# Optimization experiments

Hardware: AMD Instinct MI355X
Metric: run time of the kernel (lower is better)

The kernel has to match this reference:

```python
import jax, jax.numpy as jnp
import numpy as np

B, S, E, H = 2, 2048, 1024, 16
D = E // H


def setup_inputs() -> dict:
    key = jax.random.key(0)
    ks = jax.random.split(key, 8)
    q = jax.random.normal(ks[0], (B, S, E), dtype=jnp.float32)
    k = jax.random.normal(ks[1], (B, S, E), dtype=jnp.float32)
    v = jax.random.normal(ks[2], (B, S, E), dtype=jnp.float32)
    mask = jax.random.randint(ks[3], (B, 1, 1, S), 0, 2, dtype=jnp.int32)
    sc = 1.0 / np.sqrt(E)
    W_qkv = jax.random.normal(ks[4], (3 * E, E), dtype=jnp.float32) * sc
    b_qkv = jnp.zeros((3 * E,), dtype=jnp.float32)
    W_out = jax.random.normal(ks[5], (E, E), dtype=jnp.float32) * sc
    b_out = jnp.zeros((E,), dtype=jnp.float32)
    return {"q": q, "k": k, "v": v, "mask": mask,
            "W_qkv": W_qkv, "b_qkv": b_qkv, "W_out": W_out, "b_out": b_out}


def reference(q, k, v, mask, W_qkv, b_qkv, W_out, b_out):
    # Fused qkv linear: q takes the Q-slice, k the K-slice, v the V-slice.
    qp = (q @ W_qkv[:E].T + b_qkv[:E]).reshape(B, S, H, D)
    kp = (k @ W_qkv[E:2 * E].T + b_qkv[E:2 * E]).reshape(B, S, H, D)
    vp = (v @ W_qkv[2 * E:].T + b_qkv[2 * E:]).reshape(B, S, H, D)
    # (B,H,S,S) scores -- NOTE: original module does NOT scale by sqrt(d)
    energy = jnp.einsum('nqhd,nkhd->nhqk', qp, kp)
    energy = jnp.where(mask == 0, jnp.float32(-1e20), energy)
    attention = jax.nn.softmax(energy, axis=-1)
    out = jnp.einsum('nhql,nlhd->nqhd', attention, vp).reshape(B, S, E)
    return out @ W_out.T + b_out
```

## Files before the change

### kernel.cpp

```cpp
#include <hip/hip_runtime.h>
#include <stdint.h>

constexpr int B_ = 2, S_ = 2048, E_ = 1024, H_ = 16, D_ = 64;
constexpr int M_ = B_ * S_;

typedef unsigned short u16;
typedef __attribute__((ext_vector_type(8))) short short8;
typedef __attribute__((ext_vector_type(4))) float f32x4;

__device__ __forceinline__ u16 f2bf(float f) {
  uint32_t u = __float_as_uint(f);
  return (u16)((u + 0x7FFFu + ((u >> 16) & 1u)) >> 16);
}
__device__ __forceinline__ void tsplit(float x, u16& hi, u16& lo) {
  const uint32_t u = __float_as_uint(x);
  hi = (u16)(u >> 16);
  const float hif = __uint_as_float(u & 0xFFFF0000u);
  lo = (u16)(__float_as_uint(x - hif) >> 16);
}

__device__ __forceinline__ void block_sync() {
  asm volatile("s_waitcnt lgkmcnt(0)" ::: "memory");
  __builtin_amdgcn_s_barrier();
}

__global__ __launch_bounds__(256) void split_f32_kernel(
    const float* __restrict__ src, u16* __restrict__ hi, u16* __restrict__ lo, int n4)
{
  const int i = blockIdx.x * 256 + threadIdx.x;
  if (i >= n4) return;
  const float4 x = ((const float4*)src)[i];
  ushort4 h, l;
  tsplit(x.x, h.x, l.x); tsplit(x.y, h.y, l.y);
  tsplit(x.z, h.z, l.z); tsplit(x.w, h.w, l.w);
  ((ushort4*)hi)[i] = h;
  ((ushort4*)lo)[i] = l;
}

__global__ __launch_bounds__(256) void mask_scan_kernel(
    const int* __restrict__ mask, int* __restrict__ opos, int* __restrict__ nk)
{
  __shared__ int tmp[256];
  __shared__ int coff;
  const int b = blockIdx.x, t = threadIdx.x;
  for (int c = t; c < S_; c += 256) opos[b * S_ + c] = 0;
  if (t == 0) coff = 0;
  __syncthreads();
  for (int c = 0; c < S_; c += 256) {
    const int m = (mask[b * S_ + c + t] != 0) ? 1 : 0;
    int x = m;
    tmp[t] = x;
    __syncthreads();
#pragma unroll
    for (int off = 1; off < 256; off <<= 1) {
      const int v = (t >= off) ? tmp[t - off] : 0;
      __syncthreads();
      x += v;
      tmp[t] = x;
      __syncthreads();
    }
    const int base = coff;
    if (m) opos[b * S_ + base + x - 1] = c + t;
    __syncthreads();
    if (t == 255) coff = base + x;
    __syncthreads();
  }
  if (t == 0) nk[b] = coff;
}

__global__ __launch_bounds__(256) void gemm_qkv_kernel(
    const float* __restrict__ q, const float* __restrict__ k, const float* __restrict__ v,
    const u16* __restrict__ WHi, const u16* __restrict__ WLo,
    const float* __restrict__ bias,
    const int* __restrict__ Opos, const int* __restrict__ NkArr,
    u16* __restrict__ QpHi, u16* __restrict__ QpLo,
    u16* __restrict__ KpHi, u16* __restrict__ KpLo,
    u16* __restrict__ Vp)
{
  __shared__ __align__(16) short smem[15360];
  short* Ah = smem;
  short* Al = smem + 5120;
  short* Bh = smem + 10240;
  short* Bl = smem + 12800;

  const int t = threadIdx.x;
  const int m0 = blockIdx.x * 128;
  const int n0g = blockIdx.y * 64;
  const int proj = n0g >> 10;
  const int nloc = n0g & (E_ - 1);
  const bool split = (proj < 2);
  const int bb = m0 >> 11, mloc = m0 & (S_ - 1);
  const int nkb = NkArr[bb];
  if (proj != 0 && mloc >= nkb) return;

  const float* A = (proj == 0) ? q : (proj == 1) ? k : v;

  const int w = t >> 6, lane = t & 63;
  const int g = lane >> 4, lc = lane & 15;
  const int wm = w & 1, wn = w >> 1;
  const int sra = t >> 1, sca = (t & 1) * 16;
  const int srb = t >> 2, scb = (t & 3) * 8;

  int arow;
  if (proj == 0) arow = m0 + sra;
  else arow = bb * S_ + (Opos[bb * S_ + mloc + sra] & (S_ - 1));
  const float* Abp = A + (size_t)arow * E_ + sca;
  const u16* Bhb = WHi + (size_t)(n0g + srb) * E_ + scb;
  const u16* Blb = WLo + (size_t)(n0g + srb) * E_ + scb;

  f32x4 acc[4][2];
#pragma unroll
  for (int i = 0; i < 4; ++i)
#pragma unroll
    for (int j = 0; j < 2; ++j) acc[i][j] = (f32x4){0.f, 0.f, 0.f, 0.f};

  auto loadA = [&](float4* ar, int kk) {
#pragma unroll
    for (int i = 0; i < 4; ++i) ar[i] = *(const float4*)(Abp + kk + 4 * i);
  };
  auto writeA = [&](const float4* ar) {
    ushort hh[16], ll[16];
#pragma unroll
    for (int i = 0; i < 4; ++i) {
      tsplit(ar[i].x, hh[4 * i + 0], ll[4 * i + 0]);
      tsplit(ar[i].y, hh[4 * i + 1], ll[4 * i + 1]);
      tsplit(ar[i].z, hh[4 * i + 2], ll[4 * i + 2]);
      tsplit(ar[i].w, hh[4 * i + 3], ll[4 * i + 3]);
    }
    *(short8*)&Ah[sra * 40 + sca]     = *(const short8*)&hh[0];
    *(short8*)&Ah[sra * 40 + sca + 8] = *(const short8*)&hh[8];
    if (split) {
      *(short8*)&Al[sra * 40 + sca]     = *(const short8*)&ll[0];
      *(short8*)&Al[sra * 40 + sca + 8] = *(const short8*)&ll[8];
    }
  };

  float4 arP[2][4];
  short8 brP[2], crP[2] = {};
  loadA(arP[0], 0);
  loadA(arP[1], 32);
  brP[0] = *(const short8*)(Bhb);
  brP[1] = *(const short8*)(Bhb + 32);
  if (split) {
    crP[0] = *(const short8*)(Blb);
    crP[1] = *(const short8*)(Blb + 32);
  }

#pragma unroll 2
  for (int k0 = 0; k0 < E_; k0 += 32) {
    const int p = (k0 >> 5) & 1;
    block_sync();
    writeA(arP[p]);
    *(short8*)&Bh[srb * 40 + scb] = brP[p];
    if (split) *(short8*)&Bl[srb * 40 + scb] = crP[p];
    block_sync();
    {
      const int kk = (k0 + 64) & (E_ - 1);
      loadA(arP[p], kk);
      brP[p] = *(const short8*)(Bhb + kk);
      if (split) crP[p] = *(const short8*)(Blb + kk);
    }

    short8 ah[4], al[4], bh[2], bl[2];
#pragma unroll
    for (int mt = 0; mt < 4; ++mt) {
      const int ro = (wm * 64 + mt * 16 + lc) * 40 + g * 8;
      ah[mt] = *(const short8*)&Ah[ro];
      if (split) al[mt] = *(const short8*)&Al[ro];
    }
#pragma unroll
    for (int nt = 0; nt < 2; ++nt) {
      const int ro = (wn * 32 + nt * 16 + lc) * 40 + g * 8;
      bh[nt] = *(const short8*)&Bh[ro];
      if (split) bl[nt] = *(const short8*)&Bl[ro];
    }
#pragma unroll
    for (int mt = 0; mt < 4; ++mt)
#pragma unroll
      for (int nt = 0; nt < 2; ++nt) {
        f32x4 a = acc[mt][nt];
        a = __builtin_amdgcn_mfma_f32_16x16x32_bf16(ah[mt], bh[nt], a, 0, 0, 0);
        if (split) {
          a = __builtin_amdgcn_mfma_f32_16x16x32_bf16(ah[mt], bl[nt], a, 0, 0, 0);
          a = __builtin_amdgcn_mfma_f32_16x16x32_bf16(al[mt], bh[nt], a, 0, 0, 0);
        }
        acc[mt][nt] = a;
      }
  }

  float bs[2];
#pragma unroll
  for (int nt = 0; nt < 2; ++nt) bs[nt] = bias[n0g + wn * 32 + nt * 16 + lc];

  if (proj < 2) {
    u16* Hi = (proj == 0) ? QpHi : KpHi;
    u16* Lo = (proj == 0) ? QpLo : KpLo;
    const int head = nloc >> 6;
    short* T = smem + w * 2560;
    const int s = (m0 + wm * 64 + lane) & (S_ - 1);
    const size_t rowb = (((size_t)(bb * H_ + head)) * S_ + s) * D_ + wn * 32;
#pragma unroll
    for (int pass = 0; pass < 2; ++pass) {
      __syncthreads();
#pragma unroll
      for (int nt = 0; nt < 2; ++nt)
#pragma unroll
        for (int mt = 0; mt < 4; ++mt)
#pragma unroll
          for (int r = 0; r < 4; ++r) {
            const float val = acc[mt][nt][r] + bs[nt];
            const uint32_t u = __float_as_uint(val);
            u16 x;
            if (pass == 0) x = (u16)(u >> 16);
            else {
              const float hif = __uint_as_float(u & 0xFFFF0000u);
              x = (u16)(__float_as_uint(val - hif) >> 16);
            }
            T[(mt * 16 + g * 4 + r) * 40 + nt * 16 + lc] = (short)x;
          }
      __syncthreads();
      u16* dst = (pass == 0) ? Hi : Lo;
#pragma unroll
      for (int j = 0; j < 4; ++j)
        *(short8*)&dst[rowb + 8 * j] = *(const short8*)&T[lane * 40 + 8 * j];
    }
  } else {
#pragma unroll
    for (int mt = 0; mt < 4; ++mt) {
      const int jb = mloc + wm * 64 + mt * 16 + g * 4;
#pragma unroll
      for (int nt = 0; nt < 2; ++nt) {
        const int nE = nloc + wn * 32 + nt * 16 + lc;
        const int h = nE >> 6, d = nE & 63;
        const size_t rb = (((size_t)(bb * H_ + h)) * D_ + d) * S_;
#pragma unroll
        for (int r = 0; r < 4; ++r) {
          if (jb + r < nkb) Vp[rb + jb + r] = f2bf(acc[mt][nt][r] + bs[nt]);
        }
      }
    }
  }
}

__global__ __launch_bounds__(256, 4) void attn_mfma_kernel(
    const u16* __restrict__ QpHi, const u16* __restrict__ QpLo,
    const u16* __restrict__ KpHi, const u16* __restrict__ KpLo,
    const u16* __restrict__ Vp,
    const int* __restrict__ nkArr,
    u16* __restrict__ AOHi)
{
  __shared__ __align__(16) short sm[18432];
  short* Khi = sm;
  short* Klo = sm + 4608;
  short* Vt  = sm + 9216;
  short* Pb  = sm + 13824;

  const int t = threadIdx.x;
  const int w = t >> 6, lane = t & 63;
  const int g = lane >> 4, lc = lane & 15;
  const int bh = blockIdx.y;
  const int b = bh >> 4, hh = bh & 15;
  const int q0 = blockIdx.x * 64;
  const size_t hb = (size_t)bh * S_ * D_;
  const u16* QgH = QpHi + hb;
  const u16* QgL = QpLo + hb;
  const u16* KgH = KpHi + hb;
  const u16* KgL = KpLo + hb;
  const u16* Vg  = Vp + hb;
  short* Pw = Pb + w * 1152;

  const int nk = nkArr[b];
  const int kend = ((nk + 63) >> 6) << 6;

  short8 qh[2], ql[2];
  {
    const size_t base = (size_t)(q0 + 16 * w + lc) * D_ + 8 * g;
    qh[0] = *(const short8*)&QgH[base];
    qh[1] = *(const short8*)&QgH[base + 32];
    ql[0] = *(const short8*)&QgL[base];
    ql[1] = *(const short8*)&QgL[base + 32];
  }

  short8 ones8 = {0, 0, 0, 0, 0, 0, 0, 0};
  if (lc == 0) {
    const short o = (short)0x3F80;
    ones8 = (short8){o, o, o, o, o, o, o, o};
  }

  f32x4 O[4];
  f32x4 Ol = (f32x4){0.f, 0.f, 0.f, 0.f};
#pragma unroll
  for (int dt = 0; dt < 4; ++dt) O[dt] = (f32x4){0.f, 0.f, 0.f, 0.f};
  float mst[4] = {-INFINITY, -INFINITY, -INFINITY, -INFINITY};

  const int srow = t >> 2, sc16 = (t & 3) * 16;

  short8 kr[2], lr[2], vr[2];
  kr[0] = *(const short8*)&KgH[srow * D_ + sc16];
  kr[1] = *(const short8*)&KgH[srow * D_ + sc16 + 8];
  lr[0] = *(const short8*)&KgL[srow * D_ + sc16];
  lr[1] = *(const short8*)&KgL[srow * D_ + sc16 + 8];
  vr[0] = *(const short8*)&Vg[srow * S_ + sc16];
  vr[1] = *(const short8*)&Vg[srow * S_ + sc16 + 8];

  for (int kt = 0; kt < kend; kt += 64) {
    block_sync();
    *(short8*)&Khi[srow * 72 + sc16]     = kr[0];
    *(short8*)&Khi[srow * 72 + sc16 + 8] = kr[1];
    *(short8*)&Klo[srow * 72 + sc16]     = lr[0];
    *(short8*)&Klo[srow * 72 + sc16 + 8] = lr[1];
    *(short8*)&Vt[srow * 72 + sc16]      = vr[0];
    *(short8*)&Vt[srow * 72 + sc16 + 8]  = vr[1];
    block_sync();
    if (kt + 64 < kend) {
      const int kn = kt + 64;
      kr[0] = *(const short8*)&KgH[(kn + srow) * D_ + sc16];
      kr[1] = *(const short8*)&KgH[(kn + srow) * D_ + sc16 + 8];
      lr[0] = *(const short8*)&KgL[(kn + srow) * D_ + sc16];
      lr[1] = *(const short8*)&KgL[(kn + srow) * D_ + sc16 + 8];
      vr[0] = *(const short8*)&Vg[srow * S_ + kn + sc16];
      vr[1] = *(const short8*)&Vg[srow * S_ + kn + sc16 + 8];
    }

    f32x4 sc[4];
#pragma unroll
    for (int kt16 = 0; kt16 < 4; ++kt16) {
      const int ko = (16 * kt16 + lc) * 72 + 8 * g;
      const short8 kh0 = *(const short8*)&Khi[ko];
      const short8 kh1 = *(const short8*)&Khi[ko + 32];
      const short8 kl0 = *(const short8*)&Klo[ko];
      const short8 kl1 = *(const short8*)&Klo[ko + 32];
      f32x4 a = {0.f, 0.f, 0.f, 0.f};
      a = __builtin_amdgcn_mfma_f32_16x16x32_bf16(qh[0], kh0, a, 0, 0, 0);
      a = __builtin_amdgcn_mfma_f32_16x16x32_bf16(qh[1], kh1, a, 0, 0, 0);
      a = __builtin_amdgcn_mfma_f32_16x16x32_bf16(qh[0], kl0, a, 0, 0, 0);
      a = __builtin_amdgcn_mfma_f32_16x16x32_bf16(qh[1], kl1, a, 0, 0, 0);
      a = __builtin_amdgcn_mfma_f32_16x16x32_bf16(ql[0], kh0, a, 0, 0, 0);
      a = __builtin_amdgcn_mfma_f32_16x16x32_bf16(ql[1], kh1, a, 0, 0, 0);
      sc[kt16] = a;
    }

    if (kt + 64 > nk) {
#pragma unroll
      for (int kt16 = 0; kt16 < 4; ++kt16) {
        if (kt + 16 * kt16 + lc >= nk) {
          sc[kt16][0] = -1e20f; sc[kt16][1] = -1e20f;
          sc[kt16][2] = -1e20f; sc[kt16][3] = -1e20f;
        }
      }
    }

    float al[4];
#pragma unroll
    for (int r = 0; r < 4; ++r) {
      float vv = fmaxf(fmaxf(sc[0][r], sc[1][r]), fmaxf(sc[2][r], sc[3][r]));
      vv = fmaxf(vv, __shfl_xor(vv, 1));
      vv = fmaxf(vv, __shfl_xor(vv, 2));
      vv = fmaxf(vv, __shfl_xor(vv, 4));
      vv = fmaxf(vv, __shfl_xor(vv, 8));
      const float mn = fmaxf(mst[r], vv);
      al[r] = __expf(mst[r] - mn);
      mst[r] = mn;
    }
#pragma unroll
    for (int kt16 = 0; kt16 < 4; ++kt16) {
#pragma unroll
      for (int r = 0; r < 4; ++r)
        sc[kt16][r] = __expf(sc[kt16][r] - mst[r]);
    }
    const f32x4 alv = {al[0], al[1], al[2], al[3]};
    O[0] *= alv; O[1] *= alv; O[2] *= alv; O[3] *= alv;
    Ol *= alv;
#pragma unroll
    for (int kt16 = 0; kt16 < 4; ++kt16) {
#pragma unroll
      for (int r = 0; r < 4; ++r)
        Pw[(4 * g + r) * 72 + 16 * kt16 + lc] = (short)f2bf(sc[kt16][r]);
    }

    short8 pa[2];
    pa[0] = *(const short8*)&Pw[lc * 72 + 8 * g];
    pa[1] = *(const short8*)&Pw[lc * 72 + 32 + 8 * g];
    Ol = __builtin_amdgcn_mfma_f32_16x16x32_bf16(pa[0], ones8, Ol, 0, 0, 0);
    Ol = __builtin_amdgcn_mfma_f32_16x16x32_bf16(pa[1], ones8, Ol, 0, 0, 0);
#pragma unroll
    for (int dt = 0; dt < 4; ++dt) {
      const int vo = (16 * dt + lc) * 72 + 8 * g;
      const short8 vb0 = *(const short8*)&Vt[vo];
      const short8 vb1 = *(const short8*)&Vt[vo + 32];
      O[dt] = __builtin_amdgcn_mfma_f32_16x16x32_bf16(pa[0], vb0, O[dt], 0, 0, 0);
      O[dt] = __builtin_amdgcn_mfma_f32_16x16x32_bf16(pa[1], vb1, O[dt], 0, 0, 0);
    }
  }

#pragma unroll
  for (int r = 0; r < 4; ++r) {
    const float lv = __shfl(Ol[r], lane & 48);
    const float lir = 1.0f / lv;
    const int qrow = q0 + 16 * w + 4 * g + r;
    const size_t rowb = (size_t)(b * S_ + qrow) * E_ + hh * 64;
#pragma unroll
    for (int dt = 0; dt < 4; ++dt)
      AOHi[rowb + dt * 16 + lc] = f2bf(O[dt][r] * lir);
  }
}

__global__ __launch_bounds__(256) void gemm_out_kernel(
    const u16* __restrict__ AHi,
    const u16* __restrict__ WHi,
    const float* __restrict__ bias, float* __restrict__ out)
{
  __shared__ __align__(16) short smem[5120];
  short* Ah = smem;
  short* Bh = smem + 2560;

  const int t = threadIdx.x;
  const int m0 = blockIdx.x * 64;
  const int n0 = blockIdx.y * 64;
  const int w = t >> 6, lane = t & 63;
  const int g = lane >> 4, lc = lane & 15;
  const int wm = w & 1, wn = w >> 1;
  const int sr = t >> 2, sc = (t & 3) * 8;

  const u16* Ahb = AHi + (size_t)(m0 + sr) * E_ + sc;
  const u16* Bhb = WHi + (size_t)(n0 + sr) * E_ + sc;

  f32x4 acc[2][2];
#pragma unroll
  for (int i = 0; i < 2; ++i)
#pragma unroll
    for (int j = 0; j < 2; ++j) acc[i][j] = (f32x4){0.f, 0.f, 0.f, 0.f};

  short8 arP[2], brP[2];
  arP[0] = *(const short8*)(Ahb);
  arP[1] = *(const short8*)(Ahb + 32);
  brP[0] = *(const short8*)(Bhb);
  brP[1] = *(const short8*)(Bhb + 32);

#pragma unroll 2
  for (int k0 = 0; k0 < E_; k0 += 32) {
    const int p = (k0 >> 5) & 1;
    block_sync();
    *(short8*)&Ah[sr * 40 + sc] = arP[p];
    *(short8*)&Bh[sr * 40 + sc] = brP[p];
    block_sync();
    {
      const int kk = (k0 + 64) & (E_ - 1);
      arP[p] = *(const short8*)(Ahb + kk);
      brP[p] = *(const short8*)(Bhb + kk);
    }

    short8 ah[2], bh[2];
#pragma unroll
    for (int mt = 0; mt < 2; ++mt)
      ah[mt] = *(const short8*)&Ah[(wm * 32 + mt * 16 + lc) * 40 + g * 8];
#pragma unroll
    for (int nt = 0; nt < 2; ++nt)
      bh[nt] = *(const short8*)&Bh[(wn * 32 + nt * 16 + lc) * 40 + g * 8];
#pragma unroll
    for (int mt = 0; mt < 2; ++mt)
#pragma unroll
      for (int nt = 0; nt < 2; ++nt)
        acc[mt][nt] = __builtin_amdgcn_mfma_f32_16x16x32_bf16(ah[mt], bh[nt], acc[mt][nt], 0, 0, 0);
  }

  float bs[2];
#pragma unroll
  for (int nt = 0; nt < 2; ++nt) bs[nt] = bias[n0 + wn * 32 + nt * 16 + lc];
#pragma unroll
  for (int nt = 0; nt < 2; ++nt) {
    const int nc = n0 + wn * 32 + nt * 16 + lc;
#pragma unroll
    for (int mt = 0; mt < 2; ++mt) {
#pragma unroll
      for (int r = 0; r < 4; ++r) {
        const int mrow = m0 + wm * 32 + mt * 16 + g * 4 + r;
        out[(size_t)mrow * E_ + nc] = acc[mt][nt][r] + bs[nt];
      }
    }
  }
}

extern "C" void kernel_launch(void* const* d_in, const int* in_sizes, int n_in,
                              void* d_out, int out_size, void* d_ws, size_t ws_size,
                              hipStream_t stream) {
  const float* q    = (const float*)d_in[0];
  const float* k    = (const float*)d_in[1];
  const float* v    = (const float*)d_in[2];
  const int*   mask = (const int*)d_in[3];
  const float* Wqkv = (const float*)d_in[4];
  const float* bqkv = (const float*)d_in[5];
  const float* Wout = (const float*)d_in[6];
  const float* bout = (const float*)d_in[7];
  float* out = (float*)d_out;

  char* wsb = (char*)d_ws;
  u16* WqkvHi = (u16*)(wsb + 0);
  u16* WqkvLo = (u16*)(wsb + 6291456);
  u16* WoutHi = (u16*)(wsb + 12582912);
  int* Opos   = (int*)(wsb + 14680064);
  int* Nk     = (int*)(wsb + 14680064 + 16384);
  u16* WoutLo = (u16*)(wsb + 14680064);
  u16* QpHi   = (u16*)(wsb + 16777216);
  u16* QpLo   = (u16*)(wsb + 25165824);
  u16* KpHi   = (u16*)(wsb + 33554432);
  u16* KpLo   = (u16*)(wsb + 41943040);
  u16* Vp     = (u16*)(wsb + 50331648);
  u16* AOHi   = (u16*)(wsb + 58720256);

  hipLaunchKernelGGL(split_f32_kernel, dim3(3072), dim3(256), 0, stream,
                     Wqkv, WqkvHi, WqkvLo, 786432);
  hipLaunchKernelGGL(split_f32_kernel, dim3(1024), dim3(256), 0, stream,
                     Wout, WoutHi, WoutLo, 262144);
  hipLaunchKernelGGL(mask_scan_kernel, dim3(B_), dim3(256), 0, stream,
                     mask, Opos, Nk);
  hipMemsetAsync(Vp, 0, 8388608, stream);
  hipLaunchKernelGGL(gemm_qkv_kernel, dim3(M_ / 128, 48), dim3(256), 0, stream,
                     q, k, v, WqkvHi, WqkvLo, bqkv, Opos, Nk,
                     QpHi, QpLo, KpHi, KpLo, Vp);
  hipLaunchKernelGGL(attn_mfma_kernel, dim3(S_ / 64, B_ * H_), dim3(256), 0, stream,
                     QpHi, QpLo, KpHi, KpLo, Vp, Nk, AOHi);
  hipLaunchKernelGGL(gemm_out_kernel, dim3(M_ / 64, E_ / 64), dim3(256), 0, stream,
                     AOHi, WoutHi, bout, out);
}
```

Baseline: 296.6 us.

## Double-buffer LDS tiles in all GEMMs and attention, widen attention blocks to 512 threads

Each of the three kernels (QKV GEMM, attention, output GEMM) now keeps two LDS buffers. The next tile is written into the alternate buffer while the current one is consumed, so only one barrier is needed per k-step instead of two. The attention kernel also moves to 512-thread blocks covering 128 query rows, so one K/V tile load is shared by eight waves. In exchange, LDS use per block doubles, which may reduce occupancy, and the 512-thread launch bound with min 4 blocks may put pressure on registers.

```diff
diff --git a/kernel.cpp b/kernel.cpp
--- a/kernel.cpp
+++ b/kernel.cpp
@@ -77,11 +77,7 @@
     u16* __restrict__ KpHi, u16* __restrict__ KpLo,
     u16* __restrict__ Vp)
 {
-  __shared__ __align__(16) short smem[15360];
-  short* Ah = smem;
-  short* Al = smem + 5120;
-  short* Bh = smem + 10240;
-  short* Bl = smem + 12800;
+  __shared__ __align__(16) short smem[30720];
 
   const int t = threadIdx.x;
   const int m0 = blockIdx.x * 128;
@@ -118,7 +114,11 @@
 #pragma unroll
     for (int i = 0; i < 4; ++i) ar[i] = *(const float4*)(Abp + kk + 4 * i);
   };
-  auto writeA = [&](const float4* ar) {
+  auto writeAB = [&](const float4* ar, short8 br, short8 cr, int pb) {
+    short* Ah = smem + pb * 15360;
+    short* Al = Ah + 5120;
+    short* Bh = Ah + 10240;
+    short* Bl = Ah + 12800;
     ushort hh[16], ll[16];
 #pragma unroll
     for (int i = 0; i < 4; ++i) {
@@ -129,50 +129,48 @@
     }
     *(short8*)&Ah[sra * 40 + sca]     = *(const short8*)&hh[0];
     *(short8*)&Ah[sra * 40 + sca + 8] = *(const short8*)&hh[8];
+    *(short8*)&Bh[srb * 40 + scb]     = br;
     if (split) {
       *(short8*)&Al[sra * 40 + sca]     = *(const short8*)&ll[0];
       *(short8*)&Al[sra * 40 + sca + 8] = *(const short8*)&ll[8];
+      *(short8*)&Bl[srb * 40 + scb]     = cr;
     }
   };
 
-  float4 arP[2][4];
-  short8 brP[2], crP[2] = {};
-  loadA(arP[0], 0);
-  loadA(arP[1], 32);
-  brP[0] = *(const short8*)(Bhb);
-  brP[1] = *(const short8*)(Bhb + 32);
-  if (split) {
-    crP[0] = *(const short8*)(Blb);
-    crP[1] = *(const short8*)(Blb + 32);
-  }
-
-#pragma unroll 2
+  float4 ar[4]; short8 br = {}, cr = {};
+  loadA(ar, 0);
+  br = *(const short8*)(Bhb);
+  if (split) cr = *(const short8*)(Blb);
+  writeAB(ar, br, cr, 0);
+  loadA(ar, 32);
+  br = *(const short8*)(Bhb + 32);
+  if (split) cr = *(const short8*)(Blb + 32);
+
   for (int k0 = 0; k0 < E_; k0 += 32) {
     const int p = (k0 >> 5) & 1;
+    const short* Ahp = smem + p * 15360;
+    const short* Alp = Ahp + 5120;
+    const short* Bhp = Ahp + 10240;
+    const short* Blp = Ahp + 12800;
     block_sync();
-    writeA(arP[p]);
-    *(short8*)&Bh[srb * 40 + scb] = brP[p];
-    if (split) *(short8*)&Bl[srb * 40 + scb] = crP[p];
-    block_sync();
-    {
-      const int kk = (k0 + 64) & (E_ - 1);
-      loadA(arP[p], kk);
-      brP[p] = *(const short8*)(Bhb + kk);
-      if (split) crP[p] = *(const short8*)(Blb + kk);
-    }
-
     short8 ah[4], al[4], bh[2], bl[2];
 #pragma unroll
     for (int mt = 0; mt < 4; ++mt) {
       const int ro = (wm * 64 + mt * 16 + lc) * 40 + g * 8;
-      ah[mt] = *(const short8*)&Ah[ro];
-      if (split) al[mt] = *(const short8*)&Al[ro];
+      ah[mt] = *(const short8*)&Ahp[ro];
+      if (split) al[mt] = *(const short8*)&Alp[ro];
     }
 #pragma unroll
     for (int nt = 0; nt < 2; ++nt) {
       const int ro = (wn * 32 + nt * 16 + lc) * 40 + g * 8;
-      bh[nt] = *(const short8*)&Bh[ro];
-      if (split) bl[nt] = *(const short8*)&Bl[ro];
+      bh[nt] = *(const short8*)&Bhp[ro];
+      if (split) bl[nt] = *(const short8*)&Blp[ro];
+    }
+    if (k0 + 32 < E_) writeAB(ar, br, cr, p ^ 1);
+    if (k0 + 64 < E_) {
+      loadA(ar, k0 + 64);
+      br = *(const short8*)(Bhb + k0 + 64);
+      if (split) cr = *(const short8*)(Blb + k0 + 64);
     }
 #pragma unroll
     for (int mt = 0; mt < 4; ++mt)
@@ -242,32 +240,28 @@
   }
 }
 
-__global__ __launch_bounds__(256, 4) void attn_mfma_kernel(
+__global__ __launch_bounds__(512, 4) void attn_mfma_kernel(
     const u16* __restrict__ QpHi, const u16* __restrict__ QpLo,
     const u16* __restrict__ KpHi, const u16* __restrict__ KpLo,
     const u16* __restrict__ Vp,
     const int* __restrict__ nkArr,
     u16* __restrict__ AOHi)
 {
-  __shared__ __align__(16) short sm[18432];
-  short* Khi = sm;
-  short* Klo = sm + 4608;
-  short* Vt  = sm + 9216;
-  short* Pb  = sm + 13824;
+  __shared__ __align__(16) short sm[36864];
 
   const int t = threadIdx.x;
   const int w = t >> 6, lane = t & 63;
   const int g = lane >> 4, lc = lane & 15;
   const int bh = blockIdx.y;
   const int b = bh >> 4, hh = bh & 15;
-  const int q0 = blockIdx.x * 64;
+  const int q0 = blockIdx.x * 128;
   const size_t hb = (size_t)bh * S_ * D_;
   const u16* QgH = QpHi + hb;
   const u16* QgL = QpLo + hb;
   const u16* KgH = KpHi + hb;
   const u16* KgL = KpLo + hb;
   const u16* Vg  = Vp + hb;
-  short* Pw = Pb + w * 1152;
+  short* Pw = sm + 27648 + w * 1152;
 
   const int nk = nkArr[b];
   const int kend = ((nk + 63) >> 6) << 6;
@@ -293,34 +287,33 @@
   for (int dt = 0; dt < 4; ++dt) O[dt] = (f32x4){0.f, 0.f, 0.f, 0.f};
   float mst[4] = {-INFINITY, -INFINITY, -INFINITY, -INFINITY};
 
-  const int srow = t >> 2, sc16 = (t & 3) * 16;
-
-  short8 kr[2], lr[2], vr[2];
-  kr[0] = *(const short8*)&KgH[srow * D_ + sc16];
-  kr[1] = *(const short8*)&KgH[srow * D_ + sc16 + 8];
-  lr[0] = *(const short8*)&KgL[srow * D_ + sc16];
-  lr[1] = *(const short8*)&KgL[srow * D_ + sc16 + 8];
-  vr[0] = *(const short8*)&Vg[srow * S_ + sc16];
-  vr[1] = *(const short8*)&Vg[srow * S_ + sc16 + 8];
+  const int srow = t >> 3, sc8 = (t & 7) * 8;
+
+  short8 kr, lr, vr;
+  auto loadT = [&](int kt) {
+    kr = *(const short8*)&KgH[(kt + srow) * D_ + sc8];
+    lr = *(const short8*)&KgL[(kt + srow) * D_ + sc8];
+    vr = *(const short8*)&Vg[srow * S_ + kt + sc8];
+  };
+  auto writeT = [&](int pb) {
+    short* base = sm + pb * 13824;
+    *(short8*)&base[srow * 72 + sc8]        = kr;
+    *(short8*)&base[4608 + srow * 72 + sc8] = lr;
+    *(short8*)&base[9216 + srow * 72 + sc8] = vr;
+  };
+
+  loadT(0);
+  writeT(0);
+  if (64 < kend) loadT(64);
 
   for (int kt = 0; kt < kend; kt += 64) {
+    const int p = (kt >> 6) & 1;
+    const short* Khi = sm + p * 13824;
+    const short* Klo = Khi + 4608;
+    const short* Vt  = Khi + 9216;
     block_sync();
-    *(short8*)&Khi[srow * 72 + sc16]     = kr[0];
-    *(short8*)&Khi[srow * 72 + sc16 + 8] = kr[1];
-    *(short8*)&Klo[srow * 72 + sc16]     = lr[0];
-    *(short8*)&Klo[srow * 72 + sc16 + 8] = lr[1];
-    *(short8*)&Vt[srow * 72 + sc16]      = vr[0];
-    *(short8*)&Vt[srow * 72 + sc16 + 8]  = vr[1];
-    block_sync();
-    if (kt + 64 < kend) {
-      const int kn = kt + 64;
-      kr[0] = *(const short8*)&KgH[(kn + srow) * D_ + sc16];
-      kr[1] = *(const short8*)&KgH[(kn + srow) * D_ + sc16 + 8];
-      lr[0] = *(const short8*)&KgL[(kn + srow) * D_ + sc16];
-      lr[1] = *(const short8*)&KgL[(kn + srow) * D_ + sc16 + 8];
-      vr[0] = *(const short8*)&Vg[srow * S_ + kn + sc16];
-      vr[1] = *(const short8*)&Vg[srow * S_ + kn + sc16 + 8];
-    }
+    if (kt + 64 < kend) writeT(p ^ 1);
+    if (kt + 128 < kend) loadT(kt + 128);
 
     f32x4 sc[4];
 #pragma unroll
@@ -410,9 +403,7 @@
     const u16* __restrict__ WHi,
     const float* __restrict__ bias, float* __restrict__ out)
 {
-  __shared__ __align__(16) short smem[5120];
-  short* Ah = smem;
-  short* Bh = smem + 2560;
+  __shared__ __align__(16) short smem[10240];
 
   const int t = threadIdx.x;
   const int m0 = blockIdx.x * 64;
@@ -431,25 +422,19 @@
 #pragma unroll
     for (int j = 0; j < 2; ++j) acc[i][j] = (f32x4){0.f, 0.f, 0.f, 0.f};
 
-  short8 arP[2], brP[2];
-  arP[0] = *(const short8*)(Ahb);
-  arP[1] = *(const short8*)(Ahb + 32);
-  brP[0] = *(const short8*)(Bhb);
-  brP[1] = *(const short8*)(Bhb + 32);
-
-#pragma unroll 2
+  short8 arr, brr;
+  arr = *(const short8*)(Ahb);
+  brr = *(const short8*)(Bhb);
+  *(short8*)&smem[sr * 40 + sc]        = arr;
+  *(short8*)&smem[2560 + sr * 40 + sc] = brr;
+  arr = *(const short8*)(Ahb + 32);
+  brr = *(const short8*)(Bhb + 32);
+
   for (int k0 = 0; k0 < E_; k0 += 32) {
     const int p = (k0 >> 5) & 1;
+    const short* Ah = smem + p * 5120;
+    const short* Bh = Ah + 2560;
     block_sync();
-    *(short8*)&Ah[sr * 40 + sc] = arP[p];
-    *(short8*)&Bh[sr * 40 + sc] = brP[p];
-    block_sync();
-    {
-      const int kk = (k0 + 64) & (E_ - 1);
-      arP[p] = *(const short8*)(Ahb + kk);
-      brP[p] = *(const short8*)(Bhb + kk);
-    }
-
     short8 ah[2], bh[2];
 #pragma unroll
     for (int mt = 0; mt < 2; ++mt)
@@ -457,6 +442,15 @@
 #pragma unroll
     for (int nt = 0; nt < 2; ++nt)
       bh[nt] = *(const short8*)&Bh[(wn * 32 + nt * 16 + lc) * 40 + g * 8];
+    if (k0 + 32 < E_) {
+      short* AhN = smem + (p ^ 1) * 5120;
+      *(short8*)&AhN[sr * 40 + sc]        = arr;
+      *(short8*)&AhN[2560 + sr * 40 + sc] = brr;
+    }
+    if (k0 + 64 < E_) {
+      arr = *(const short8*)(Ahb + k0 + 64);
+      brr = *(const short8*)(Bhb + k0 + 64);
+    }
 #pragma unroll
     for (int mt = 0; mt < 2; ++mt)
 #pragma unroll
@@ -518,7 +512,7 @@
   hipLaunchKernelGGL(gemm_qkv_kernel, dim3(M_ / 128, 48), dim3(256), 0, stream,
                      q, k, v, WqkvHi, WqkvLo, bqkv, Opos, Nk,
                      QpHi, QpLo, KpHi, KpLo, Vp);
-  hipLaunchKernelGGL(attn_mfma_kernel, dim3(S_ / 64, B_ * H_), dim3(256), 0, stream,
+  hipLaunchKernelGGL(attn_mfma_kernel, dim3(S_ / 128, B_ * H_), dim3(512), 0, stream,
                      QpHi, QpLo, KpHi, KpLo, Vp, Nk, AOHi);
   hipLaunchKernelGGL(gemm_out_kernel, dim3(M_ / 64, E_ / 64), dim3(256), 0, stream,
                      AOHi, WoutHi, bout, out);
```

Result: no change. 296.0 us (-0.2%).

## Widen QKV GEMM tile to 128 columns and simplify register prefetch

Applied to the files above, without the earlier changes.

The QKV projection GEMM now computes a 128x128 output tile per block instead of 128x64, halving the grid in N. Each converted fp32 A tile is therefore reused across twice as many columns, so the hi/lo split of A is done half as often. The two-deep register double buffer is replaced by a single-stage prefetch. The epilogue staging buffer is widened to match. The larger accumulator set raises register pressure and may cut occupancy, and the shallower prefetch may hide less load latency. The K/Q output row index for K is also changed to the compacted row index.

```diff
diff --git a/kernel.cpp b/kernel.cpp
--- a/kernel.cpp
+++ b/kernel.cpp
@@ -77,15 +77,15 @@
     u16* __restrict__ KpHi, u16* __restrict__ KpLo,
     u16* __restrict__ Vp)
 {
-  __shared__ __align__(16) short smem[15360];
+  __shared__ __align__(16) short smem[20480];
   short* Ah = smem;
   short* Al = smem + 5120;
   short* Bh = smem + 10240;
-  short* Bl = smem + 12800;
+  short* Bl = smem + 15360;
 
   const int t = threadIdx.x;
   const int m0 = blockIdx.x * 128;
-  const int n0g = blockIdx.y * 64;
+  const int n0g = blockIdx.y * 128;
   const int proj = n0g >> 10;
   const int nloc = n0g & (E_ - 1);
   const bool split = (proj < 2);
@@ -98,70 +98,62 @@
   const int w = t >> 6, lane = t & 63;
   const int g = lane >> 4, lc = lane & 15;
   const int wm = w & 1, wn = w >> 1;
-  const int sra = t >> 1, sca = (t & 1) * 16;
-  const int srb = t >> 2, scb = (t & 3) * 8;
+  const int srow = t >> 1, sh = (t & 1) * 16;
 
   int arow;
-  if (proj == 0) arow = m0 + sra;
-  else arow = bb * S_ + (Opos[bb * S_ + mloc + sra] & (S_ - 1));
-  const float* Abp = A + (size_t)arow * E_ + sca;
-  const u16* Bhb = WHi + (size_t)(n0g + srb) * E_ + scb;
-  const u16* Blb = WLo + (size_t)(n0g + srb) * E_ + scb;
-
-  f32x4 acc[4][2];
+  if (proj == 0) arow = m0 + srow;
+  else arow = bb * S_ + (Opos[bb * S_ + mloc + srow] & (S_ - 1));
+  const float* Ab = A + (size_t)arow * E_ + sh;
+  const u16* Bhb = WHi + (size_t)(n0g + srow) * E_ + sh;
+  const u16* Blb = WLo + (size_t)(n0g + srow) * E_ + sh;
+
+  f32x4 acc[4][4];
 #pragma unroll
   for (int i = 0; i < 4; ++i)
 #pragma unroll
-    for (int j = 0; j < 2; ++j) acc[i][j] = (f32x4){0.f, 0.f, 0.f, 0.f};
-
-  auto loadA = [&](float4* ar, int kk) {
-#pragma unroll
-    for (int i = 0; i < 4; ++i) ar[i] = *(const float4*)(Abp + kk + 4 * i);
-  };
-  auto writeA = [&](const float4* ar) {
-    ushort hh[16], ll[16];
-#pragma unroll
-    for (int i = 0; i < 4; ++i) {
-      tsplit(ar[i].x, hh[4 * i + 0], ll[4 * i + 0]);
-      tsplit(ar[i].y, hh[4 * i + 1], ll[4 * i + 1]);
-      tsplit(ar[i].z, hh[4 * i + 2], ll[4 * i + 2]);
-      tsplit(ar[i].w, hh[4 * i + 3], ll[4 * i + 3]);
-    }
-    *(short8*)&Ah[sra * 40 + sca]     = *(const short8*)&hh[0];
-    *(short8*)&Ah[sra * 40 + sca + 8] = *(const short8*)&hh[8];
+    for (int j = 0; j < 4; ++j) acc[i][j] = (f32x4){0.f, 0.f, 0.f, 0.f};
+
+  float4 ar[4]; short8 br[2], cr[2];
+#pragma unroll
+  for (int i = 0; i < 4; ++i) ar[i] = *(const float4*)(Ab + 4 * i);
+  br[0] = *(const short8*)(Bhb);     br[1] = *(const short8*)(Bhb + 8);
+  if (split) { cr[0] = *(const short8*)(Blb); cr[1] = *(const short8*)(Blb + 8); }
+
+  for (int k0 = 0; k0 < E_; k0 += 32) {
+    __syncthreads();
+    {
+      ushort hh[16], ll[16];
+#pragma unroll
+      for (int i = 0; i < 4; ++i) {
+        tsplit(ar[i].x, hh[4 * i + 0], ll[4 * i + 0]);
+        tsplit(ar[i].y, hh[4 * i + 1], ll[4 * i + 1]);
+        tsplit(ar[i].z, hh[4 * i + 2], ll[4 * i + 2]);
+        tsplit(ar[i].w, hh[4 * i + 3], ll[4 * i + 3]);
+      }
+      *(short8*)&Ah[srow * 40 + sh]     = *(const short8*)&hh[0];
+      *(short8*)&Ah[srow * 40 + sh + 8] = *(const short8*)&hh[8];
+      if (split) {
+        *(short8*)&Al[srow * 40 + sh]     = *(const short8*)&ll[0];
+        *(short8*)&Al[srow * 40 + sh + 8] = *(const short8*)&ll[8];
+      }
+    }
+    *(short8*)&Bh[srow * 40 + sh]     = br[0];
+    *(short8*)&Bh[srow * 40 + sh + 8] = br[1];
     if (split) {
-      *(short8*)&Al[sra * 40 + sca]     = *(const short8*)&ll[0];
-      *(short8*)&Al[sra * 40 + sca + 8] = *(const short8*)&ll[8];
-    }
-  };
-
-  float4 arP[2][4];
-  short8 brP[2], crP[2] = {};
-  loadA(arP[0], 0);
-  loadA(arP[1], 32);
-  brP[0] = *(const short8*)(Bhb);
-  brP[1] = *(const short8*)(Bhb + 32);
-  if (split) {
-    crP[0] = *(const short8*)(Blb);
-    crP[1] = *(const short8*)(Blb + 32);
-  }
-
-#pragma unroll 2
-  for (int k0 = 0; k0 < E_; k0 += 32) {
-    const int p = (k0 >> 5) & 1;
-    block_sync();
-    writeA(arP[p]);
-    *(short8*)&Bh[srb * 40 + scb] = brP[p];
-    if (split) *(short8*)&Bl[srb * 40 + scb] = crP[p];
-    block_sync();
-    {
-      const int kk = (k0 + 64) & (E_ - 1);
-      loadA(arP[p], kk);
-      brP[p] = *(const short8*)(Bhb + kk);
-      if (split) crP[p] = *(const short8*)(Blb + kk);
-    }
-
-    short8 ah[4], al[4], bh[2], bl[2];
+      *(short8*)&Bl[srow * 40 + sh]     = cr[0];
+      *(short8*)&Bl[srow * 40 + sh + 8] = cr[1];
+    }
+    __syncthreads();
+    if (k0 + 32 < E_) {
+#pragma unroll
+      for (int i = 0; i < 4; ++i) ar[i] = *(const float4*)(Ab + k0 + 32 + 4 * i);
+      br[0] = *(const short8*)(Bhb + k0 + 32); br[1] = *(const short8*)(Bhb + k0 + 40);
+      if (split) {
+        cr[0] = *(const short8*)(Blb + k0 + 32); cr[1] = *(const short8*)(Blb + k0 + 40);
+      }
+    }
+
+    short8 ah[4], al[4], bh[4], bl[4];
 #pragma unroll
     for (int mt = 0; mt < 4; ++mt) {
       const int ro = (wm * 64 + mt * 16 + lc) * 40 + g * 8;
@@ -169,15 +161,15 @@
       if (split) al[mt] = *(const short8*)&Al[ro];
     }
 #pragma unroll
-    for (int nt = 0; nt < 2; ++nt) {
-      const int ro = (wn * 32 + nt * 16 + lc) * 40 + g * 8;
+    for (int nt = 0; nt < 4; ++nt) {
+      const int ro = (wn * 64 + nt * 16 + lc) * 40 + g * 8;
       bh[nt] = *(const short8*)&Bh[ro];
       if (split) bl[nt] = *(const short8*)&Bl[ro];
     }
 #pragma unroll
     for (int mt = 0; mt < 4; ++mt)
 #pragma unroll
-      for (int nt = 0; nt < 2; ++nt) {
+      for (int nt = 0; nt < 4; ++nt) {
         f32x4 a = acc[mt][nt];
         a = __builtin_amdgcn_mfma_f32_16x16x32_bf16(ah[mt], bh[nt], a, 0, 0, 0);
         if (split) {
@@ -188,22 +180,23 @@
       }
   }
 
-  float bs[2];
-#pragma unroll
-  for (int nt = 0; nt < 2; ++nt) bs[nt] = bias[n0g + wn * 32 + nt * 16 + lc];
+  float bs[4];
+#pragma unroll
+  for (int nt = 0; nt < 4; ++nt) bs[nt] = bias[n0g + wn * 64 + nt * 16 + lc];
 
   if (proj < 2) {
     u16* Hi = (proj == 0) ? QpHi : KpHi;
     u16* Lo = (proj == 0) ? QpLo : KpLo;
-    const int head = nloc >> 6;
-    short* T = smem + w * 2560;
-    const int s = (m0 + wm * 64 + lane) & (S_ - 1);
-    const size_t rowb = (((size_t)(bb * H_ + head)) * S_ + s) * D_ + wn * 32;
+    const int hwave = (nloc + wn * 64) >> 6;
+    short* T = smem + w * 4608;
+    const int srow_out = (proj == 0) ? ((m0 + wm * 64 + lane) & (S_ - 1))
+                                     : (mloc + wm * 64 + lane);
+    const size_t rowb = (((size_t)(bb * H_ + hwave)) * S_ + srow_out) * D_;
 #pragma unroll
     for (int pass = 0; pass < 2; ++pass) {
       __syncthreads();
 #pragma unroll
-      for (int nt = 0; nt < 2; ++nt)
+      for (int nt = 0; nt < 4; ++nt)
 #pragma unroll
         for (int mt = 0; mt < 4; ++mt)
 #pragma unroll
@@ -216,21 +209,21 @@
               const float hif = __uint_as_float(u & 0xFFFF0000u);
               x = (u16)(__float_as_uint(val - hif) >> 16);
             }
-            T[(mt * 16 + g * 4 + r) * 40 + nt * 16 + lc] = (short)x;
+            T[(mt * 16 + g * 4 + r) * 72 + nt * 16 + lc] = (short)x;
           }
       __syncthreads();
       u16* dst = (pass == 0) ? Hi : Lo;
 #pragma unroll
-      for (int j = 0; j < 4; ++j)
-        *(short8*)&dst[rowb + 8 * j] = *(const short8*)&T[lane * 40 + 8 * j];
+      for (int j = 0; j < 8; ++j)
+        *(short8*)&dst[rowb + 8 * j] = *(const short8*)&T[lane * 72 + 8 * j];
     }
   } else {
 #pragma unroll
     for (int mt = 0; mt < 4; ++mt) {
       const int jb = mloc + wm * 64 + mt * 16 + g * 4;
 #pragma unroll
-      for (int nt = 0; nt < 2; ++nt) {
-        const int nE = nloc + wn * 32 + nt * 16 + lc;
+      for (int nt = 0; nt < 4; ++nt) {
+        const int nE = nloc + wn * 64 + nt * 16 + lc;
         const int h = nE >> 6, d = nE & 63;
         const size_t rb = (((size_t)(bb * H_ + h)) * D_ + d) * S_;
 #pragma unroll
@@ -515,7 +508,7 @@
   hipLaunchKernelGGL(mask_scan_kernel, dim3(B_), dim3(256), 0, stream,
                      mask, Opos, Nk);
   hipMemsetAsync(Vp, 0, 8388608, stream);
-  hipLaunchKernelGGL(gemm_qkv_kernel, dim3(M_ / 128, 48), dim3(256), 0, stream,
+  hipLaunchKernelGGL(gemm_qkv_kernel, dim3(M_ / 128, 24), dim3(256), 0, stream,
                      q, k, v, WqkvHi, WqkvLo, bqkv, Opos, Nk,
                      QpHi, QpLo, KpHi, KpLo, Vp);
   hipLaunchKernelGGL(attn_mfma_kernel, dim3(S_ / 64, B_ * H_), dim3(256), 0, stream,
```

Measured after the change: 294.0 us. About the same (-0.9%).
